# Kernel optimization log

Measured on AMD Instinct MI355X. Metric: run time of the kernel, lower is better.

The kernel has to match this reference:

```python
import jax, jax.numpy as jnp
from jax import lax
import numpy as np

DN = ('NCHW', 'OIHW', 'NCHW')


def conv3x3(x, w, b):
    y = lax.conv_general_dilated(x, w, (1, 1), ((1, 1), (1, 1)), dimension_numbers=DN)
    return y + b[None, :, None, None]


def box_mean(x, k):
    # Uniform k x k box mean with reflect padding; separable (exactly equal to
    # the dense ones/k^2 conv in the original since the kernel is rank-1).
    pad = k // 2
    C = x.shape[1]
    xp = jnp.pad(x, ((0, 0), (0, 0), (pad, pad), (pad, pad)), mode='reflect')
    kh = jnp.ones((C, 1, k, 1), x.dtype) / k
    kw = jnp.ones((C, 1, 1, k), x.dtype) / k
    y = lax.conv_general_dilated(xp, kh, (1, 1), 'VALID', feature_group_count=C, dimension_numbers=DN)
    y = lax.conv_general_dilated(y, kw, (1, 1), 'VALID', feature_group_count=C, dimension_numbers=DN)
    return y


def std_map_for_window(features, k):
    # features: [N, 8, H, W]
    C = features.shape[1]
    m = box_mean(features, k)
    m2 = box_mean(features * features, k)
    var = jnp.maximum(m2 - m * m, 1e-6)
    w = jax.nn.softmax(jnp.ones((C,), features.dtype))  # uniform (C==8 branch)
    sm = jnp.einsum('nchw,c->nhw', jnp.sqrt(var), w)[:, None]  # [N,1,H,W]
    return jnp.power(sm, 0.8)


def setup_inputs() -> dict:
    key = jax.random.key(0)
    ks = jax.random.split(key, 8)
    B, H, W = 8, 512, 512
    x = jax.random.normal(ks[0], (B, 4, H, W), dtype=jnp.float32)
    s = 0.05
    conv1_w = jax.random.normal(ks[1], (32, 4, 3, 3), jnp.float32) * s
    conv1_b = jnp.zeros((32,), jnp.float32)
    conv2_w = jax.random.normal(ks[2], (16, 32, 3, 3), jnp.float32) * s
    conv2_b = jnp.zeros((16,), jnp.float32)
    conv3_w = jax.random.normal(ks[3], (8, 16, 3, 3), jnp.float32) * s
    conv3_b = jnp.zeros((8,), jnp.float32)
    fusion_w = jnp.full((1, 3, 1, 1), 1.0 / 3.0, jnp.float32)  # init per module
    fusion_b = jnp.zeros((1,), jnp.float32)
    channel_weights = jnp.ones((4,), jnp.float32) / 4.0
    return dict(x=x, conv1_w=conv1_w, conv1_b=conv1_b, conv2_w=conv2_w,
                conv2_b=conv2_b, conv3_w=conv3_w, conv3_b=conv3_b,
                fusion_w=fusion_w, fusion_b=fusion_b,
                channel_weights=channel_weights)


def reference(x, conv1_w, conv1_b, conv2_w, conv2_b, conv3_w, conv3_b,
              fusion_w, fusion_b, channel_weights):
    window_sizes = (11, 25, 49)
    # feature extractor
    f = jax.nn.leaky_relu(conv3x3(x, conv1_w, conv1_b), 0.2)
    f = jax.nn.leaky_relu(conv3x3(f, conv2_w, conv2_b), 0.2)
    f = conv3x3(f, conv3_w, conv3_b)  # [B,8,H,W]
    # multi-scale std maps
    maps = [std_map_for_window(f, k) for k in window_sizes]
    multi = jnp.concatenate(maps, axis=1)  # [B,3,H,W]
    fused = jax.nn.relu(
        lax.conv_general_dilated(multi, fusion_w, (1, 1), 'VALID', dimension_numbers=DN)
        + fusion_b[None, :, None, None])  # [B,1,H,W]
    # adaptive thresholds
    std_flat = fused.ravel()
    q = jnp.quantile(std_flat, jnp.array([0.25, 0.75], fused.dtype))
    q25, q75 = q[0], q[1]
    iqr = q75 - q25
    iqr = jnp.where(iqr < 1e-5, jnp.asarray(0.05, fused.dtype), iqr)
    global_std = jnp.std(x, axis=(2, 3), keepdims=True, ddof=1)  # [B,4,1,1]
    lower = jnp.broadcast_to((q25 - 0.5 * iqr), global_std.shape)
    upper = jnp.broadcast_to((q75 + 0.5 * iqr), global_std.shape)
    gf = jnp.clip(global_std * 5.0, 0.5, 2.0)
    lower = lower * gf
    upper = upper * gf
    cw = jax.nn.softmax(channel_weights).reshape(1, 4, 1, 1)
    channel_std = jnp.std(x * cw, axis=(2, 3), keepdims=True, ddof=1)
    cf = jnp.clip(channel_std * 2.0, 0.8, 1.2)
    lower = lower * cf
    upper = upper * cf
    degenerate = jnp.min(jnp.abs(upper - lower)) < 1e-5
    mean_t = (upper + lower) / 2
    lower = jnp.where(degenerate, mean_t - 0.05, lower)
    upper = jnp.where(degenerate, mean_t + 0.05, upper)
    # texture mask
    diff = jnp.maximum(upper - lower, 1e-5)
    norm = jnp.clip((fused - lower) / diff, 0.0, 1.0)  # [B,4,H,W] via broadcast
    mask = jax.nn.sigmoid(6.0 * norm - 3.0)
    return jnp.mean(mask, axis=1, keepdims=True)  # [B,1,H,W]
```

## Files before the change

### kernel.cpp

```cpp
#include <hip/hip_runtime.h>
#include <hip/hip_bf16.h>
#include <math.h>


__global__ __launch_bounds__(256, 2) void conv12_k(
    const float* __restrict__ x,
    const float* __restrict__ w1,
    const float* __restrict__ b1,
    const float* __restrict__ w2,
    const float* __restrict__ b2,
    float* __restrict__ f2)
{
    __shared__ float xs[4 * 36 * 68];
    __shared__ float f1s[4 * 34 * 68];

    const int t  = threadIdx.x;
    const int tx = t & 7;
    const int ty = t >> 3;
    const int x0 = blockIdx.x * 64;
    const int y0 = blockIdx.y * 32;
    const int bb = blockIdx.z;
    const float* xb = x + (size_t)bb * 4 * 262144;

    for (int i = t; i < 9792; i += 256) {
        int ci  = i / 2448;
        int rem = i - ci * 2448;
        int r   = rem / 68;
        int c   = rem - r * 68;
        int Y = y0 - 2 + r, X = x0 - 2 + c;
        float v = 0.f;
        if ((unsigned)Y < 512u && (unsigned)X < 512u)
            v = xb[ci * 262144 + Y * 512 + X];
        xs[i] = v;
    }

    float acc[16][8];
#pragma unroll
    for (int j = 0; j < 16; ++j)
#pragma unroll
        for (int p = 0; p < 8; ++p) acc[j][p] = 0.f;

    for (int g = 0; g < 8; ++g) {
        __syncthreads();

        {
            const int g4 = g * 4;
            for (int it = t; it < 578; it += 256) {
                int r  = it / 17;
                int q  = it - r * 17;
                int c0 = q * 4;
                int Y1 = y0 - 1 + r;
                float v[4][4];
#pragma unroll
                for (int fc = 0; fc < 4; ++fc) {
                    float b = b1[g4 + fc];
                    v[fc][0] = b; v[fc][1] = b; v[fc][2] = b; v[fc][3] = b;
                }
#pragma unroll
                for (int ci = 0; ci < 4; ++ci) {
#pragma unroll
                    for (int ky = 0; ky < 3; ++ky) {
                        const float* xr = &xs[ci * 2448 + (r + ky) * 68 + c0];
                        float4 a  = *(const float4*)xr;
                        float2 bl = *(const float2*)(xr + 4);
                        float rr[6] = {a.x, a.y, a.z, a.w, bl.x, bl.y};
#pragma unroll
                        for (int fc = 0; fc < 4; ++fc) {
#pragma unroll
                            for (int kx = 0; kx < 3; ++kx) {
                                float w = w1[(g4 + fc) * 36 + ci * 9 + ky * 3 + kx];
#pragma unroll
                                for (int p = 0; p < 4; ++p)
                                    v[fc][p] = fmaf(rr[p + kx], w, v[fc][p]);
                            }
                        }
                    }
                }
                bool rowok = ((unsigned)Y1 < 512u);
#pragma unroll
                for (int fc = 0; fc < 4; ++fc) {
                    float st[4];
#pragma unroll
                    for (int p = 0; p < 4; ++p) {
                        int X1 = x0 - 1 + c0 + p;
                        bool ok = rowok && ((unsigned)X1 < 512u) && (c0 + p <= 65);
                        float tv = v[fc][p];
                        tv = tv > 0.f ? tv : 0.2f * tv;
                        st[p] = ok ? tv : 0.f;
                    }
                    *(float4*)&f1s[fc * 2312 + r * 68 + c0] =
                        make_float4(st[0], st[1], st[2], st[3]);
                }
            }
        }
        __syncthreads();

#pragma unroll
        for (int fc = 0; fc < 4; ++fc) {
            const int ci = g * 4 + fc;
#pragma unroll
            for (int dy = 0; dy < 3; ++dy) {
                const float* rowp = &f1s[fc * 2312 + (ty + dy) * 68 + tx * 8];
                float4 a0 = *(const float4*)(rowp);
                float4 a1 = *(const float4*)(rowp + 4);
                float2 a2 = *(const float2*)(rowp + 8);
                float rr[10] = {a0.x, a0.y, a0.z, a0.w,
                                a1.x, a1.y, a1.z, a1.w, a2.x, a2.y};
#pragma unroll
                for (int j = 0; j < 16; ++j) {
#pragma unroll
                    for (int dx = 0; dx < 3; ++dx) {
                        float w = w2[(j * 32 + ci) * 9 + dy * 3 + dx];
#pragma unroll
                        for (int p = 0; p < 8; ++p)
                            acc[j][p] = fmaf(rr[p + dx], w, acc[j][p]);
                    }
                }
            }
        }
    }

    const int y = y0 + ty;
#pragma unroll
    for (int j = 0; j < 16; ++j) {
        float b = b2[j];
        float* op = f2 + (((size_t)bb * 16 + j) * 512 + y) * 512 + x0 + tx * 8;
        float v[8];
#pragma unroll
        for (int p = 0; p < 8; ++p) {
            float tv = acc[j][p] + b;
            v[p] = tv > 0.f ? tv : 0.2f * tv;
        }
        ((float4*)op)[0] = make_float4(v[0], v[1], v[2], v[3]);
        ((float4*)op)[1] = make_float4(v[4], v[5], v[6], v[7]);
    }
}

__global__ __launch_bounds__(256) void conv3_k(
    const float* __restrict__ in,
    const float* __restrict__ wgt,
    const float* __restrict__ bias,
    float* __restrict__ out)
{
    constexpr int TW = 64, TH = 32, SW = TW + 4;
    __shared__ float sl[(TH + 2) * SW];

    const int tx = threadIdx.x & 7;
    const int ty = threadIdx.x >> 3;
    const int x0 = blockIdx.x * TW;
    const int y0 = blockIdx.y * TH;
    const int bb = blockIdx.z;

    const float* inb = in + (size_t)bb * 16 * 262144;

    float acc[8][8];
#pragma unroll
    for (int j = 0; j < 8; ++j)
#pragma unroll
        for (int p = 0; p < 8; ++p) acc[j][p] = 0.f;

    for (int ci = 0; ci < 16; ++ci) {
        __syncthreads();
        const float* ip = inb + (size_t)ci * 262144;
        for (int idx = threadIdx.x; idx < (TH + 2) * (TW + 2); idx += 256) {
            int r  = idx / (TW + 2);
            int cc = idx - r * (TW + 2);
            int yy = y0 - 1 + r, xx = x0 - 1 + cc;
            float v = 0.f;
            if ((unsigned)yy < 512u && (unsigned)xx < 512u) v = ip[yy * 512 + xx];
            sl[r * SW + cc] = v;
        }
        __syncthreads();
        const float* wci = wgt + (size_t)ci * 9;
#pragma unroll
        for (int dy = 0; dy < 3; ++dy) {
            const float* rowp = &sl[(ty + dy) * SW + tx * 8];
            float4 a0 = *(const float4*)(rowp);
            float4 a1 = *(const float4*)(rowp + 4);
            float2 a2 = *(const float2*)(rowp + 8);
            float rr[10] = {a0.x, a0.y, a0.z, a0.w,
                            a1.x, a1.y, a1.z, a1.w, a2.x, a2.y};
#pragma unroll
            for (int j = 0; j < 8; ++j) {
#pragma unroll
                for (int dx = 0; dx < 3; ++dx) {
                    float w = wci[(size_t)j * 16 * 9 + dy * 3 + dx];
#pragma unroll
                    for (int p = 0; p < 8; ++p)
                        acc[j][p] = fmaf(rr[p + dx], w, acc[j][p]);
                }
            }
        }
    }

    const int y = y0 + ty;
#pragma unroll
    for (int j = 0; j < 8; ++j) {
        float b = bias[j];
        float* op = out + (((size_t)bb * 8 + j) * 512 + y) * 512 + x0 + tx * 8;
        float v[8];
#pragma unroll
        for (int p = 0; p < 8; ++p) v[p] = acc[j][p] + b;
        ((float4*)op)[0] = make_float4(v[0], v[1], v[2], v[3]);
        ((float4*)op)[1] = make_float4(v[4], v[5], v[6], v[7]);
    }
}

__device__ __forceinline__ float2 f2add(float2 a, float2 b) {
    return make_float2(a.x + b.x, a.y + b.y);
}
__device__ __forceinline__ int mir(int v) {
    return v < 0 ? -v : (v > 511 ? 1022 - v : v);
}

#define YB 4

__global__ __launch_bounds__(256) void stdmap_k(
    const float* __restrict__ f,
    const float* __restrict__ fw,
    const float* __restrict__ fbp,
    float* __restrict__ fused,
    int b0)
{
    const int total = gridDim.x * gridDim.y;
    const int lin   = blockIdx.y * gridDim.x + blockIdx.x;
    const int task  = (lin & 7) * (total >> 3) + (lin >> 3);
    const int bb    = task >> 7;
    const int y0    = (task & 127) * YB;
    const int t    = threadIdx.x;
    const int lane = t & 63, wid = t >> 6;

    __shared__ float S[3][2][513];
    __shared__ float wtt[4][6];

    const int   RAD[3] = {5, 12, 24};
    const float INV[3] = {1.f/121.f, 1.f/625.f, 1.f/2401.f};

    float smacc[3][YB][2];
#pragma unroll
    for (int sc = 0; sc < 3; ++sc)
#pragma unroll
        for (int yy = 0; yy < YB; ++yy)
            { smacc[sc][yy][0] = 0.f; smacc[sc][yy][1] = 0.f; }

    for (int c = 0; c < 8; ++c) {
        const float* base = f + ((size_t)bb * 8 + c) * 512 * 512;

        float2 wf[3], wq[3];
        {
            float2 sf[3] = {{0.f,0.f},{0.f,0.f},{0.f,0.f}};
            float2 sq[3] = {{0.f,0.f},{0.f,0.f},{0.f,0.f}};
#pragma unroll
            for (int dy = -24; dy <= 24; ++dy) {
                int row = mir(y0 + dy);
                float2 v  = ((const float2*)(base + (size_t)row * 512))[t];
                float2 vq = make_float2(v.x * v.x, v.y * v.y);
                int ad = dy < 0 ? -dy : dy;
                int ring = ad <= 5 ? 0 : (ad <= 12 ? 1 : 2);
                sf[ring] = f2add(sf[ring], v);
                sq[ring] = f2add(sq[ring], vq);
            }
            wf[0] = sf[0];               wq[0] = sq[0];
            wf[1] = f2add(sf[1], wf[0]); wq[1] = f2add(sq[1], wq[0]);
            wf[2] = f2add(sf[2], wf[1]); wq[2] = f2add(sq[2], wq[1]);
        }

        for (int yy = 0; yy < YB; ++yy) {
            const int y = y0 + yy;
            if (yy > 0) {
#pragma unroll
                for (int sc = 0; sc < 3; ++sc) {
                    int ra = mir(y + RAD[sc]);
                    int rs = mir(y - 1 - RAD[sc]);
                    float2 va = ((const float2*)(base + (size_t)ra * 512))[t];
                    float2 vs = ((const float2*)(base + (size_t)rs * 512))[t];
                    wf[sc].x += va.x - vs.x;       wf[sc].y += va.y - vs.y;
                    wq[sc].x += va.x*va.x - vs.x*vs.x;
                    wq[sc].y += va.y*va.y - vs.y*vs.y;
                }
            }

            float pf[3], pq[3], incf[3], incq[3];
#pragma unroll
            for (int sc = 0; sc < 3; ++sc) {
                pf[sc] = wf[sc].x + wf[sc].y;
                pq[sc] = wq[sc].x + wq[sc].y;
                incf[sc] = pf[sc]; incq[sc] = pq[sc];
            }
#pragma unroll
            for (int off = 1; off < 64; off <<= 1) {
#pragma unroll
                for (int sc = 0; sc < 3; ++sc) {
                    float uf = __shfl_up(incf[sc], (unsigned)off, 64);
                    float uq = __shfl_up(incq[sc], (unsigned)off, 64);
                    if (lane >= off) { incf[sc] += uf; incq[sc] += uq; }
                }
            }
            if (lane == 63) {
#pragma unroll
                for (int sc = 0; sc < 3; ++sc) {
                    wtt[wid][sc]     = incf[sc];
                    wtt[wid][3 + sc] = incq[sc];
                }
            }
            __syncthreads();
            float wpf[3] = {0.f,0.f,0.f}, wpq[3] = {0.f,0.f,0.f};
#pragma unroll
            for (int w = 0; w < 4; ++w)
                if (w < wid)
#pragma unroll
                    for (int sc = 0; sc < 3; ++sc) {
                        wpf[sc] += wtt[w][sc];
                        wpq[sc] += wtt[w][3 + sc];
                    }
#pragma unroll
            for (int sc = 0; sc < 3; ++sc) {
                float exf = wpf[sc] + incf[sc] - pf[sc];
                float exq = wpq[sc] + incq[sc] - pq[sc];
                S[sc][0][2*t+1] = exf + wf[sc].x;
                S[sc][0][2*t+2] = exf + pf[sc];
                S[sc][1][2*t+1] = exq + wq[sc].x;
                S[sc][1][2*t+2] = exq + pq[sc];
            }
            if (t == 0)
#pragma unroll
                for (int sc = 0; sc < 3; ++sc)
                    { S[sc][0][0] = 0.f; S[sc][1][0] = 0.f; }
            __syncthreads();

#pragma unroll
            for (int sc = 0; sc < 3; ++sc) {
                const int r = RAD[sc];
                const float* Sf = S[sc][0];
                const float* Sq = S[sc][1];
#pragma unroll
                for (int slot = 0; slot < 2; ++slot) {
                    int xx = 2*t + slot;
                    int lo = xx - r, hi = xx + r;
                    int loc = lo < 0 ? 0 : lo;
                    int hic = hi > 511 ? 511 : hi;
                    float wfv = Sf[hic + 1] - Sf[loc];
                    float wqv = Sq[hic + 1] - Sq[loc];
                    if (lo < 0)   { wfv += Sf[r - xx + 1] - Sf[1];
                                    wqv += Sq[r - xx + 1] - Sq[1]; }
                    if (hi > 511) { wfv += Sf[511] - Sf[1022 - xx - r];
                                    wqv += Sq[511] - Sq[1022 - xx - r]; }
                    float m   = wfv * INV[sc];
                    float m2  = wqv * INV[sc];
                    float var = m2 - m * m;
                    var = var > 1e-6f ? var : 1e-6f;
                    smacc[sc][yy][slot] += sqrtf(var);
                }
            }
            __syncthreads();
        }
    }

    const float w0 = fw[0], w1 = fw[1], w2 = fw[2], b = fbp[0];
#pragma unroll
    for (int yy = 0; yy < YB; ++yy) {
        float o[2];
#pragma unroll
        for (int slot = 0; slot < 2; ++slot) {
            float m0 = powf(smacc[0][yy][slot] * 0.125f, 0.8f);
            float m1 = powf(smacc[1][yy][slot] * 0.125f, 0.8f);
            float m2 = powf(smacc[2][yy][slot] * 0.125f, 0.8f);
            float fv = w0 * m0 + w1 * m1 + w2 * m2 + b;
            o[slot] = fv > 0.f ? fv : 0.f;
        }
        ((float2*)(fused + ((size_t)(b0 + bb) * 512 + y0 + yy) * 512))[t] =
            make_float2(o[0], o[1]);
    }
}

__global__ __launch_bounds__(256) void plane_std_part_k(
    const float* __restrict__ x, double* __restrict__ part)
{
    const int plane = blockIdx.x >> 5;
    const int blk   = blockIdx.x & 31;
    const float* p = x + (size_t)plane * 262144 + (size_t)blk * 8192;
    double s = 0.0, s2 = 0.0;
    for (int i = threadIdx.x; i < 2048; i += 256) {
        float4 v = ((const float4*)p)[i];
        s  += (double)v.x + (double)v.y + (double)v.z + (double)v.w;
        s2 += (double)v.x * v.x + (double)v.y * v.y
            + (double)v.z * v.z + (double)v.w * v.w;
    }
    __shared__ double ls[256], ls2[256];
    ls[threadIdx.x] = s; ls2[threadIdx.x] = s2;
    __syncthreads();
    for (int off = 128; off > 0; off >>= 1) {
        if (threadIdx.x < off) {
            ls[threadIdx.x]  += ls[threadIdx.x + off];
            ls2[threadIdx.x] += ls2[threadIdx.x + off];
        }
        __syncthreads();
    }
    if (threadIdx.x == 0) {
        part[2 * blockIdx.x]     = ls[0];
        part[2 * blockIdx.x + 1] = ls2[0];
    }
}

__global__ void plane_std_fin_k(const double* __restrict__ part,
                                float* __restrict__ stds)
{
    const int plane = threadIdx.x;
    if (plane >= 32) return;
    double s = 0.0, s2 = 0.0;
    for (int b = 0; b < 32; ++b) {
        s  += part[2 * (plane * 32 + b)];
        s2 += part[2 * (plane * 32 + b) + 1];
    }
    const double N = 262144.0;
    double var = (s2 - s * s / N) / (N - 1.0);
    stds[plane] = (float)sqrt(var > 0.0 ? var : 0.0);
}

__global__ __launch_bounds__(256) void hist1_k(
    const float* __restrict__ fused, unsigned* __restrict__ h)
{
    __shared__ unsigned lh[4096];
    for (int i = threadIdx.x; i < 4096; i += 256) lh[i] = 0u;
    __syncthreads();
    const int base = blockIdx.x * 2048;
    for (int i = threadIdx.x; i < 2048; i += 256) {
        unsigned bits = __float_as_uint(fused[base + i]);
        atomicAdd(&lh[bits >> 20], 1u);
    }
    __syncthreads();
    for (int i = threadIdx.x; i < 4096; i += 256) {
        unsigned c = lh[i];
        if (c) atomicAdd(&h[i], c);
    }
}

__global__ __launch_bounds__(256) void select_par_k(
    const unsigned* __restrict__ h, unsigned* __restrict__ pfx,
    unsigned* __restrict__ rem, int level)
{
    const int tt = blockIdx.x;
    const int t = threadIdx.x, lane = t & 63, wid = t >> 6;
    const unsigned targets[4] = {524287u, 524288u, 1572863u, 1572864u};
    const unsigned R = (level == 1) ? targets[tt] : rem[tt];
    const unsigned* hb = (level == 1) ? h : h + tt * 4096;

    unsigned loc[16], lsum = 0;
    const uint4* hv = (const uint4*)(hb + t * 16);
#pragma unroll
    for (int i = 0; i < 4; ++i) {
        uint4 v = hv[i];
        loc[4*i]=v.x; loc[4*i+1]=v.y; loc[4*i+2]=v.z; loc[4*i+3]=v.w;
        lsum += v.x + v.y + v.z + v.w;
    }
    __shared__ unsigned warr[4];
    __shared__ unsigned rbin, rrem;
    unsigned inc = lsum;
#pragma unroll
    for (int off = 1; off < 64; off <<= 1) {
        unsigned up = __shfl_up(inc, (unsigned)off, 64);
        if (lane >= off) inc += up;
    }
    if (lane == 63) warr[wid] = inc;
    __syncthreads();
    unsigned wpre = 0;
#pragma unroll
    for (int w = 0; w < 4; ++w) if (w < wid) wpre += warr[w];
    unsigned ex = wpre + inc - lsum;
    if (R >= ex && R < ex + lsum) {
        unsigned cum = ex;
#pragma unroll
        for (int i = 0; i < 16; ++i) {
            if (cum + loc[i] > R) { rbin = (unsigned)(t * 16 + i); rrem = R - cum; break; }
            cum += loc[i];
        }
    }
    __syncthreads();
    if (t == 0) {
        if (level == 1) { pfx[tt] = rbin << 20; rem[tt] = rrem; }
        else            { pfx[tt] |= rbin << 8; rem[tt] = rrem; }
    }
}

__global__ __launch_bounds__(256) void hist2_k(
    const float* __restrict__ fused, const unsigned* __restrict__ pfx,
    unsigned* __restrict__ h2)
{
    __shared__ unsigned lh[4 * 4096];
    for (int i = threadIdx.x; i < 4 * 4096; i += 256) lh[i] = 0u;
    unsigned p0 = pfx[0] >> 20, p1 = pfx[1] >> 20,
             p2 = pfx[2] >> 20, p3 = pfx[3] >> 20;
    __syncthreads();
    const int base = blockIdx.x * 2048;
    for (int i = threadIdx.x; i < 2048; i += 256) {
        unsigned bits = __float_as_uint(fused[base + i]);
        unsigned top = bits >> 20;
        unsigned mid = (bits >> 8) & 0xFFFu;
        if (top == p0) atomicAdd(&lh[0 * 4096 + mid], 1u);
        if (top == p1) atomicAdd(&lh[1 * 4096 + mid], 1u);
        if (top == p2) atomicAdd(&lh[2 * 4096 + mid], 1u);
        if (top == p3) atomicAdd(&lh[3 * 4096 + mid], 1u);
    }
    __syncthreads();
    for (int i = threadIdx.x; i < 4 * 4096; i += 256) {
        unsigned c = lh[i];
        if (c) atomicAdd(&h2[i], c);
    }
}

__global__ __launch_bounds__(256) void hist3_k(
    const float* __restrict__ fused, const unsigned* __restrict__ pfx,
    unsigned* __restrict__ h3)
{
    __shared__ unsigned lh[4 * 256];
    for (int i = threadIdx.x; i < 4 * 256; i += 256) lh[i] = 0u;
    unsigned p0 = pfx[0] >> 8, p1 = pfx[1] >> 8,
             p2 = pfx[2] >> 8, p3 = pfx[3] >> 8;
    __syncthreads();
    const int base = blockIdx.x * 2048;
    for (int i = threadIdx.x; i < 2048; i += 256) {
        unsigned bits = __float_as_uint(fused[base + i]);
        unsigned top = bits >> 8;
        unsigned low = bits & 0xFFu;
        if (top == p0) atomicAdd(&lh[0 * 256 + low], 1u);
        if (top == p1) atomicAdd(&lh[1 * 256 + low], 1u);
        if (top == p2) atomicAdd(&lh[2 * 256 + low], 1u);
        if (top == p3) atomicAdd(&lh[3 * 256 + low], 1u);
    }
    __syncthreads();
    for (int i = threadIdx.x; i < 4 * 256; i += 256) {
        unsigned c = lh[i];
        if (c) atomicAdd(&h3[i], c);
    }
}

__device__ __forceinline__ float clampf(float v, float lo, float hi) {
    return v < lo ? lo : (v > hi ? hi : v);
}

__global__ __launch_bounds__(256) void finalize_k(
    const unsigned* __restrict__ h3,
    const unsigned* __restrict__ pfx,
    const unsigned* __restrict__ rem,
    const float* __restrict__ stds,
    const float* __restrict__ cw,
    float* __restrict__ lu)
{
    const int tt = threadIdx.x >> 6, lane = threadIdx.x & 63;
    __shared__ float vals[4];

    {
        const unsigned R = rem[tt];
        const unsigned* h = h3 + tt * 256;
        uint4 v = ((const uint4*)h)[lane];
        unsigned loc[4] = {v.x, v.y, v.z, v.w};
        unsigned lsum = v.x + v.y + v.z + v.w;
        unsigned inc = lsum;
#pragma unroll
        for (int off = 1; off < 64; off <<= 1) {
            unsigned up = __shfl_up(inc, (unsigned)off, 64);
            if (lane >= off) inc += up;
        }
        unsigned ex = inc - lsum;
        if (R >= ex && R < ex + lsum) {
            unsigned cum = ex;
#pragma unroll
            for (int i = 0; i < 4; ++i) {
                if (cum + loc[i] > R) {
                    vals[tt] = __uint_as_float(pfx[tt] | (unsigned)(lane * 4 + i));
                    break;
                }
                cum += loc[i];
            }
        }
    }
    __syncthreads();
    if (threadIdx.x != 0) return;

    float q25 = vals[0] + 0.75f * (vals[1] - vals[0]);
    float q75 = vals[2] + 0.25f * (vals[3] - vals[2]);
    float iqr = q75 - q25;
    if (iqr < 1e-5f) iqr = 0.05f;
    float lo0 = q25 - 0.5f * iqr, up0 = q75 + 0.5f * iqr;

    float mx = cw[0];
    for (int c = 1; c < 4; ++c) mx = cw[c] > mx ? cw[c] : mx;
    float e[4], se = 0.f;
    for (int c = 0; c < 4; ++c) { e[c] = expf(cw[c] - mx); se += e[c]; }

    float l[32], u[32], mind = 1e30f;
    for (int p = 0; p < 32; ++p) {
        float sd = stds[p];
        int c = p & 3;
        float gf = clampf(sd * 5.f, 0.5f, 2.f);
        float cf = clampf(sd * (e[c] / se) * 2.f, 0.8f, 1.2f);
        l[p] = lo0 * gf * cf;
        u[p] = up0 * gf * cf;
        float d = fabsf(u[p] - l[p]);
        if (d < mind) mind = d;
    }
    bool deg = mind < 1e-5f;
    for (int p = 0; p < 32; ++p) {
        float L = l[p], U = u[p];
        if (deg) { float m = 0.5f * (L + U); L = m - 0.05f; U = m + 0.05f; }
        lu[p] = L; lu[32 + p] = U;
    }
}

__global__ __launch_bounds__(256) void mask_k(
    const float* __restrict__ fused, const float* __restrict__ lu,
    float* __restrict__ out)
{
    const int b = blockIdx.y;
    const int i = blockIdx.x * 256 + threadIdx.x;
    float fv = fused[(size_t)b * 262144 + i];
    float s = 0.f;
#pragma unroll
    for (int c = 0; c < 4; ++c) {
        float L = lu[b * 4 + c], U = lu[32 + b * 4 + c];
        float d = U - L; d = d > 1e-5f ? d : 1e-5f;
        float n = (fv - L) / d;
        n = n < 0.f ? 0.f : (n > 1.f ? 1.f : n);
        s += 1.f / (1.f + expf(3.f - 6.f * n));
    }
    out[(size_t)b * 262144 + i] = 0.25f * s;
}

extern "C" void kernel_launch(void* const* d_in, const int* in_sizes, int n_in,
                              void* d_out, int out_size, void* d_ws, size_t ws_size,
                              hipStream_t stream)
{
    const float* x   = (const float*)d_in[0];
    const float* c1w = (const float*)d_in[1];
    const float* c1b = (const float*)d_in[2];
    const float* c2w = (const float*)d_in[3];
    const float* c2b = (const float*)d_in[4];
    const float* c3w = (const float*)d_in[5];
    const float* c3b = (const float*)d_in[6];
    const float* fw  = (const float*)d_in[7];
    const float* fb  = (const float*)d_in[8];
    const float* cwt = (const float*)d_in[9];
    float* out = (float*)d_out;
    char* ws = (char*)d_ws;

    const size_t PLANE = 512 * 512;

    float* fused = (float*)ws;
    size_t off = 8 * PLANE * sizeof(float);
    float* stds = (float*)(ws + off); off += 32 * 4;
    float* lu   = (float*)(ws + off); off += 64 * 4;
    off = (off + 255) & ~(size_t)255;
    unsigned* pfx = (unsigned*)(ws + off); off += 16;
    unsigned* rem = (unsigned*)(ws + off); off += 16;
    off = (off + 255) & ~(size_t)255;
    unsigned* h1 = (unsigned*)(ws + off); off += 4096 * 4;
    unsigned* h2 = (unsigned*)(ws + off); off += 4 * 4096 * 4;
    unsigned* h3 = (unsigned*)(ws + off); off += 4 * 256 * 4;
    off = (off + 255) & ~(size_t)255;
    double* part = (double*)(ws + off); off += 1024 * 2 * sizeof(double);
    off = (off + 1023) & ~(size_t)1023;

    const size_t perb = 24 * PLANE * sizeof(float);
    int nb = 8;
    while (nb > 1 && off + (size_t)nb * perb > ws_size) nb >>= 1;
    float* f2  = (float*)(ws + off);
    float* fch = f2 + (size_t)nb * 16 * PLANE;

    hipLaunchKernelGGL(plane_std_part_k, dim3(1024), dim3(256), 0, stream, x, part);
    hipLaunchKernelGGL(plane_std_fin_k,  dim3(1),    dim3(64),  0, stream, part, stds);

    for (int b0 = 0; b0 < 8; b0 += nb) {
        const float* xc = x + (size_t)b0 * 4 * PLANE;
        hipLaunchKernelGGL(conv12_k, dim3(8, 16, nb), dim3(256), 0, stream,
                           xc, c1w, c1b, c2w, c2b, f2);
        hipLaunchKernelGGL(conv3_k,  dim3(8, 16, nb), dim3(256), 0, stream,
                           f2, c3w, c3b, fch);
        hipLaunchKernelGGL(stdmap_k, dim3(512 / YB, nb), dim3(256), 0, stream,
                           fch, fw, fb, fused, b0);
    }

    hipMemsetAsync(h1, 0, (4096 + 4 * 4096 + 4 * 256) * 4, stream);
    hipLaunchKernelGGL(hist1_k,     dim3(1024), dim3(256), 0, stream, fused, h1);
    hipLaunchKernelGGL(select_par_k, dim3(4),   dim3(256), 0, stream, h1, pfx, rem, 1);
    hipLaunchKernelGGL(hist2_k,     dim3(1024), dim3(256), 0, stream, fused, pfx, h2);
    hipLaunchKernelGGL(select_par_k, dim3(4),   dim3(256), 0, stream, h2, pfx, rem, 2);
    hipLaunchKernelGGL(hist3_k,     dim3(1024), dim3(256), 0, stream, fused, pfx, h3);
    hipLaunchKernelGGL(finalize_k,  dim3(1),    dim3(256), 0, stream,
                       h3, pfx, rem, stds, cwt, lu);
    hipLaunchKernelGGL(mask_k, dim3(1024, 8), dim3(256), 0, stream, fused, lu, out);
}
```

Before: 1.095 ms.

## Use zero-padded global buffers for conv inputs and batch conv3 channel staging

Adds a kernel that copies x into zero-padded planes and another that zeroes the halo of a padded f2 buffer. conv12 then reads x straight from global memory instead of staging it in shared memory, and writes f2 into the padded layout. conv3 stages four input channels per sync with vectorized, branch-free loads instead of one channel at a time. The aim is to remove bounds checks, cut shared-memory use and reduce barriers, at the cost of two extra kernels, extra workspace, and uncached-style global reads inside conv12's inner loop.

Result: slower. 1.186 ms (+8.3%).

```diff
diff --git a/kernel.cpp b/kernel.cpp
--- a/kernel.cpp
+++ b/kernel.cpp
@@ -3,15 +3,56 @@
 #include <math.h>
 
 
+#define XP_H 516
+#define XP_W 528
+#define F2P_H 514
+#define F2P_W 528
+
+__global__ __launch_bounds__(256) void pad_x_k(
+    const float* __restrict__ x, float* __restrict__ xp, int nplanes)
+{
+    const int i = blockIdx.x * 256 + threadIdx.x;
+    const int PER = XP_H * (XP_W / 4);
+    if (i >= nplanes * PER) return;
+    const int pl  = i / PER;
+    const int rem = i - pl * PER;
+    const int r   = rem / (XP_W / 4);
+    const int q   = rem - r * (XP_W / 4);
+    float4 v = make_float4(0.f, 0.f, 0.f, 0.f);
+    if (r >= 2 && r < 514 && q >= 2 && q < 130)
+        v = ((const float4*)(x + (size_t)pl * 262144 + (size_t)(r - 2) * 512))[q - 2];
+    ((float4*)(xp + (size_t)pl * XP_H * XP_W + (size_t)r * XP_W))[q] = v;
+}
+
+__global__ __launch_bounds__(256) void zero_f2p_k(
+    float* __restrict__ f2p, int nplanes)
+{
+    const int PER = 132 + 132 + 512 * 4;
+    const int i = blockIdx.x * 256 + threadIdx.x;
+    if (i >= nplanes * PER) return;
+    const int pl = i / PER;
+    int e = i - pl * PER;
+    int r, q;
+    if (e < 132)       { r = 0;   q = e; }
+    else if (e < 264)  { r = 513; q = e - 132; }
+    else {
+        e -= 264;
+        r = 1 + (e >> 2);
+        int idx = e & 3;
+        q = idx < 2 ? idx : 128 + idx;
+    }
+    ((float4*)(f2p + (size_t)pl * F2P_H * F2P_W + (size_t)r * F2P_W))[q] =
+        make_float4(0.f, 0.f, 0.f, 0.f);
+}
+
 __global__ __launch_bounds__(256, 2) void conv12_k(
-    const float* __restrict__ x,
+    const float* __restrict__ xp,
     const float* __restrict__ w1,
     const float* __restrict__ b1,
     const float* __restrict__ w2,
     const float* __restrict__ b2,
-    float* __restrict__ f2)
-{
-    __shared__ float xs[4 * 36 * 68];
+    float* __restrict__ f2p)
+{
     __shared__ float f1s[4 * 34 * 68];
 
     const int t  = threadIdx.x;
@@ -20,19 +61,7 @@
     const int x0 = blockIdx.x * 64;
     const int y0 = blockIdx.y * 32;
     const int bb = blockIdx.z;
-    const float* xb = x + (size_t)bb * 4 * 262144;
-
-    for (int i = t; i < 9792; i += 256) {
-        int ci  = i / 2448;
-        int rem = i - ci * 2448;
-        int r   = rem / 68;
-        int c   = rem - r * 68;
-        int Y = y0 - 2 + r, X = x0 - 2 + c;
-        float v = 0.f;
-        if ((unsigned)Y < 512u && (unsigned)X < 512u)
-            v = xb[ci * 262144 + Y * 512 + X];
-        xs[i] = v;
-    }
+    const float* xpb = xp + (size_t)(bb * 4) * XP_H * XP_W;
 
     float acc[16][8];
 #pragma unroll
@@ -60,10 +89,13 @@
                 for (int ci = 0; ci < 4; ++ci) {
 #pragma unroll
                     for (int ky = 0; ky < 3; ++ky) {
-                        const float* xr = &xs[ci * 2448 + (r + ky) * 68 + c0];
-                        float4 a  = *(const float4*)xr;
-                        float2 bl = *(const float2*)(xr + 4);
-                        float rr[6] = {a.x, a.y, a.z, a.w, bl.x, bl.y};
+                        const float* xr = xpb + (size_t)ci * XP_H * XP_W
+                                        + (size_t)(y0 + r + ky) * XP_W
+                                        + x0 + 6 + c0;
+                        float2 A = *(const float2*)xr;
+                        float2 B = *(const float2*)(xr + 2);
+                        float2 C = *(const float2*)(xr + 4);
+                        float rr[6] = {A.x, A.y, B.x, B.y, C.x, C.y};
 #pragma unroll
                         for (int fc = 0; fc < 4; ++fc) {
 #pragma unroll
@@ -124,7 +156,8 @@
 #pragma unroll
     for (int j = 0; j < 16; ++j) {
         float b = b2[j];
-        float* op = f2 + (((size_t)bb * 16 + j) * 512 + y) * 512 + x0 + tx * 8;
+        float* op = f2p + ((size_t)(bb * 16 + j) * F2P_H + (y + 1)) * F2P_W
+                  + x0 + 8 + tx * 8;
         float v[8];
 #pragma unroll
         for (int p = 0; p < 8; ++p) {
@@ -137,57 +170,66 @@
 }
 
 __global__ __launch_bounds__(256) void conv3_k(
-    const float* __restrict__ in,
+    const float* __restrict__ f2p,
     const float* __restrict__ wgt,
     const float* __restrict__ bias,
     float* __restrict__ out)
 {
-    constexpr int TW = 64, TH = 32, SW = TW + 4;
-    __shared__ float sl[(TH + 2) * SW];
-
-    const int tx = threadIdx.x & 7;
-    const int ty = threadIdx.x >> 3;
-    const int x0 = blockIdx.x * TW;
-    const int y0 = blockIdx.y * TH;
+    __shared__ float sl[4 * 34 * 72];
+
+    const int t  = threadIdx.x;
+    const int tx = t & 7;
+    const int ty = t >> 3;
+    const int x0 = blockIdx.x * 64;
+    const int y0 = blockIdx.y * 32;
     const int bb = blockIdx.z;
 
-    const float* inb = in + (size_t)bb * 16 * 262144;
-
     float acc[8][8];
 #pragma unroll
     for (int j = 0; j < 8; ++j)
 #pragma unroll
         for (int p = 0; p < 8; ++p) acc[j][p] = 0.f;
 
-    for (int ci = 0; ci < 16; ++ci) {
+    for (int cg = 0; cg < 4; ++cg) {
         __syncthreads();
-        const float* ip = inb + (size_t)ci * 262144;
-        for (int idx = threadIdx.x; idx < (TH + 2) * (TW + 2); idx += 256) {
-            int r  = idx / (TW + 2);
-            int cc = idx - r * (TW + 2);
-            int yy = y0 - 1 + r, xx = x0 - 1 + cc;
-            float v = 0.f;
-            if ((unsigned)yy < 512u && (unsigned)xx < 512u) v = ip[yy * 512 + xx];
-            sl[r * SW + cc] = v;
+        for (int i = t; i < 2448; i += 256) {
+            int ch  = i / 612;
+            int rem = i - ch * 612;
+            int rr  = rem / 18;
+            int s   = rem - rr * 18;
+            const float* src = f2p
+                + ((size_t)(bb * 16 + cg * 4 + ch) * F2P_H + (y0 + rr)) * F2P_W
+                + x0;
+            float* dst = &sl[ch * 2448 + rr * 72];
+            if (s == 16)      dst[0]  = src[7];
+            else if (s == 17) dst[65] = src[72];
+            else {
+                float4 v = *(const float4*)(src + 8 + s * 4);
+                dst[4*s+1] = v.x; dst[4*s+2] = v.y;
+                dst[4*s+3] = v.z; dst[4*s+4] = v.w;
+            }
         }
         __syncthreads();
-        const float* wci = wgt + (size_t)ci * 9;
-#pragma unroll
-        for (int dy = 0; dy < 3; ++dy) {
-            const float* rowp = &sl[(ty + dy) * SW + tx * 8];
-            float4 a0 = *(const float4*)(rowp);
-            float4 a1 = *(const float4*)(rowp + 4);
-            float2 a2 = *(const float2*)(rowp + 8);
-            float rr[10] = {a0.x, a0.y, a0.z, a0.w,
-                            a1.x, a1.y, a1.z, a1.w, a2.x, a2.y};
-#pragma unroll
-            for (int j = 0; j < 8; ++j) {
-#pragma unroll
-                for (int dx = 0; dx < 3; ++dx) {
-                    float w = wci[(size_t)j * 16 * 9 + dy * 3 + dx];
-#pragma unroll
-                    for (int p = 0; p < 8; ++p)
-                        acc[j][p] = fmaf(rr[p + dx], w, acc[j][p]);
+#pragma unroll
+        for (int ci = 0; ci < 4; ++ci) {
+            const int cig = cg * 4 + ci;
+#pragma unroll
+            for (int dy = 0; dy < 3; ++dy) {
+                const float* rowp = &sl[ci * 2448 + (ty + dy) * 72 + tx * 8];
+                float4 a0 = *(const float4*)(rowp);
+                float4 a1 = *(const float4*)(rowp + 4);
+                float2 a2 = *(const float2*)(rowp + 8);
+                float rr[10] = {a0.x, a0.y, a0.z, a0.w,
+                                a1.x, a1.y, a1.z, a1.w, a2.x, a2.y};
+#pragma unroll
+                for (int j = 0; j < 8; ++j) {
+#pragma unroll
+                    for (int dx = 0; dx < 3; ++dx) {
+                        float w = wgt[((size_t)j * 16 + cig) * 9 + dy * 3 + dx];
+#pragma unroll
+                        for (int p = 0; p < 8; ++p)
+                            acc[j][p] = fmaf(rr[p + dx], w, acc[j][p]);
+                    }
                 }
             }
         }
@@ -660,21 +702,32 @@
     double* part = (double*)(ws + off); off += 1024 * 2 * sizeof(double);
     off = (off + 1023) & ~(size_t)1023;
 
-    const size_t perb = 24 * PLANE * sizeof(float);
+    const size_t xp_pb  = (size_t)4 * XP_H * XP_W;
+    const size_t f2p_pb = (size_t)16 * F2P_H * F2P_W;
+    const size_t perb = (xp_pb + f2p_pb + 8 * PLANE) * sizeof(float);
     int nb = 8;
     while (nb > 1 && off + (size_t)nb * perb > ws_size) nb >>= 1;
-    float* f2  = (float*)(ws + off);
-    float* fch = f2 + (size_t)nb * 16 * PLANE;
+    float* xp  = (float*)(ws + off);
+    float* f2p = xp + (size_t)nb * xp_pb;
+    float* fch = f2p + (size_t)nb * f2p_pb;
 
     hipLaunchKernelGGL(plane_std_part_k, dim3(1024), dim3(256), 0, stream, x, part);
     hipLaunchKernelGGL(plane_std_fin_k,  dim3(1),    dim3(64),  0, stream, part, stds);
 
     for (int b0 = 0; b0 < 8; b0 += nb) {
         const float* xc = x + (size_t)b0 * 4 * PLANE;
+        const int xplanes  = nb * 4;
+        const int f2planes = nb * 16;
+        const int padx_items = xplanes * XP_H * (XP_W / 4);
+        const int zf2_items  = f2planes * 2312;
+        hipLaunchKernelGGL(pad_x_k, dim3((padx_items + 255) / 256), dim3(256),
+                           0, stream, xc, xp, xplanes);
+        hipLaunchKernelGGL(zero_f2p_k, dim3((zf2_items + 255) / 256), dim3(256),
+                           0, stream, f2p, f2planes);
         hipLaunchKernelGGL(conv12_k, dim3(8, 16, nb), dim3(256), 0, stream,
-                           xc, c1w, c1b, c2w, c2b, f2);
+                           xp, c1w, c1b, c2w, c2b, f2p);
         hipLaunchKernelGGL(conv3_k,  dim3(8, 16, nb), dim3(256), 0, stream,
-                           f2, c3w, c3b, fch);
+                           f2p, c3w, c3b, fch);
         hipLaunchKernelGGL(stdmap_k, dim3(512 / YB, nb), dim3(256), 0, stream,
                            fch, fw, fb, fused, b0);
     }
```

## Fuse conv1, conv2 and conv3 into one tiled kernel with halo recompute

Applied to the files above, without the earlier changes.

Merges the conv1+conv2 kernel and the separate conv3 kernel into a single kernel. conv2 outputs for the tile plus a one-pixel halo stay in registers and are staged through shared memory, so the 16-channel intermediate no longer goes through global memory. The cost is recomputing the halo for conv1 and conv2 (38x72 input and 36x72 conv1 tiles), 192 accumulator registers per thread (acc[3][16][4]) and extra synchronisation, which may lower occupancy or cause spills.

New measurement: 1.591 ms. 45.3% more time.

```diff
diff --git a/kernel.cpp b/kernel.cpp
--- a/kernel.cpp
+++ b/kernel.cpp
@@ -3,72 +3,76 @@
 #include <math.h>
 
 
-__global__ __launch_bounds__(256, 2) void conv12_k(
+__global__ __launch_bounds__(256, 2) void conv123_k(
     const float* __restrict__ x,
     const float* __restrict__ w1,
     const float* __restrict__ b1,
     const float* __restrict__ w2,
     const float* __restrict__ b2,
-    float* __restrict__ f2)
-{
-    __shared__ float xs[4 * 36 * 68];
-    __shared__ float f1s[4 * 34 * 68];
+    const float* __restrict__ w3,
+    const float* __restrict__ b3,
+    float* __restrict__ fout)
+{
+    __shared__ float xs[4 * 38 * 72 + 8];
+    __shared__ float f1s[2 * 36 * 72];
 
     const int t  = threadIdx.x;
-    const int tx = t & 7;
-    const int ty = t >> 3;
-    const int x0 = blockIdx.x * 64;
-    const int y0 = blockIdx.y * 32;
+    const int tx = t & 7, ty = t >> 3;
+    const int x0 = blockIdx.x * 64, y0 = blockIdx.y * 32;
     const int bb = blockIdx.z;
     const float* xb = x + (size_t)bb * 4 * 262144;
 
-    for (int i = t; i < 9792; i += 256) {
-        int ci  = i / 2448;
-        int rem = i - ci * 2448;
-        int r   = rem / 68;
-        int c   = rem - r * 68;
-        int Y = y0 - 2 + r, X = x0 - 2 + c;
+    for (int i = t; i < 4 * 38 * 72; i += 256) {
+        int ci  = i / (38 * 72);
+        int rem = i - ci * (38 * 72);
+        int r   = rem / 72, c = rem - r * 72;
+        int Y = y0 - 3 + r, X = x0 - 4 + c;
         float v = 0.f;
         if ((unsigned)Y < 512u && (unsigned)X < 512u)
             v = xb[ci * 262144 + Y * 512 + X];
         xs[i] = v;
     }
-
-    float acc[16][8];
-#pragma unroll
-    for (int j = 0; j < 16; ++j)
-#pragma unroll
-        for (int p = 0; p < 8; ++p) acc[j][p] = 0.f;
-
-    for (int g = 0; g < 8; ++g) {
+    if (t < 8) xs[4 * 38 * 72 + t] = 0.f;
+
+    float acc[3][16][4];
+#pragma unroll
+    for (int s = 0; s < 3; ++s)
+#pragma unroll
+        for (int j = 0; j < 16; ++j)
+#pragma unroll
+            for (int p = 0; p < 4; ++p) acc[s][j][p] = 0.f;
+
+    for (int g = 0; g < 16; ++g) {
         __syncthreads();
-
-        {
-            const int g4 = g * 4;
-            for (int it = t; it < 578; it += 256) {
-                int r  = it / 17;
-                int q  = it - r * 17;
+        const int g2 = g * 2;
+
+#pragma unroll
+        for (int s = 0; s < 3; ++s) {
+            int it = t + s * 256;
+            if (it < 648) {
+                int r  = it / 18, q = it - r * 18;
                 int c0 = q * 4;
-                int Y1 = y0 - 1 + r;
-                float v[4][4];
-#pragma unroll
-                for (int fc = 0; fc < 4; ++fc) {
-                    float b = b1[g4 + fc];
+                int Y1 = y0 - 2 + r;
+                float v[2][4];
+#pragma unroll
+                for (int fc = 0; fc < 2; ++fc) {
+                    float b = b1[g2 + fc];
                     v[fc][0] = b; v[fc][1] = b; v[fc][2] = b; v[fc][3] = b;
                 }
 #pragma unroll
                 for (int ci = 0; ci < 4; ++ci) {
 #pragma unroll
                     for (int ky = 0; ky < 3; ++ky) {
-                        const float* xr = &xs[ci * 2448 + (r + ky) * 68 + c0];
-                        float4 a  = *(const float4*)xr;
-                        float2 bl = *(const float2*)(xr + 4);
-                        float rr[6] = {a.x, a.y, a.z, a.w, bl.x, bl.y};
-#pragma unroll
-                        for (int fc = 0; fc < 4; ++fc) {
+                        const float* xr = &xs[ci * 2736 + (r + ky) * 72 + c0];
+                        float2 A = *(const float2*)xr;
+                        float2 B = *(const float2*)(xr + 2);
+                        float2 C = *(const float2*)(xr + 4);
+                        float rr[6] = {A.x, A.y, B.x, B.y, C.x, C.y};
+#pragma unroll
+                        for (int fc = 0; fc < 2; ++fc) {
 #pragma unroll
                             for (int kx = 0; kx < 3; ++kx) {
-                                float w = w1[(g4 + fc) * 36 + ci * 9 + ky * 3 + kx];
+                                float w = w1[(g2 + fc) * 36 + ci * 9 + ky * 3 + kx];
 #pragma unroll
                                 for (int p = 0; p < 4; ++p)
                                     v[fc][p] = fmaf(rr[p + kx], w, v[fc][p]);
@@ -78,17 +82,16 @@
                 }
                 bool rowok = ((unsigned)Y1 < 512u);
 #pragma unroll
-                for (int fc = 0; fc < 4; ++fc) {
+                for (int fc = 0; fc < 2; ++fc) {
                     float st[4];
 #pragma unroll
                     for (int p = 0; p < 4; ++p) {
-                        int X1 = x0 - 1 + c0 + p;
-                        bool ok = rowok && ((unsigned)X1 < 512u) && (c0 + p <= 65);
+                        int X1 = x0 - 3 + c0 + p;
                         float tv = v[fc][p];
                         tv = tv > 0.f ? tv : 0.2f * tv;
-                        st[p] = ok ? tv : 0.f;
+                        st[p] = (rowok && (unsigned)X1 < 512u) ? tv : 0.f;
                     }
-                    *(float4*)&f1s[fc * 2312 + r * 68 + c0] =
+                    *(float4*)&f1s[fc * 2592 + r * 72 + c0] =
                         make_float4(st[0], st[1], st[2], st[3]);
                 }
             }
@@ -96,111 +99,104 @@
         __syncthreads();
 
 #pragma unroll
-        for (int fc = 0; fc < 4; ++fc) {
-            const int ci = g * 4 + fc;
+        for (int s = 0; s < 3; ++s) {
+            int it = t + s * 256;
+            if (it < 578) {
+                int r  = it / 17, q = it - r * 17;
+                int c0 = q * 4;
+#pragma unroll
+                for (int fc = 0; fc < 2; ++fc) {
+                    const int ciw = g2 + fc;
+#pragma unroll
+                    for (int dy = 0; dy < 3; ++dy) {
+                        const float* fp = &f1s[fc * 2592 + (r + dy) * 72 + c0];
+                        float4 A = *(const float4*)fp;
+                        float2 B = *(const float2*)(fp + 4);
+                        float rr[6] = {A.x, A.y, A.z, A.w, B.x, B.y};
+#pragma unroll
+                        for (int j = 0; j < 16; ++j) {
+#pragma unroll
+                            for (int dx = 0; dx < 3; ++dx) {
+                                float w = w2[(j * 32 + ciw) * 9 + dy * 3 + dx];
+#pragma unroll
+                                for (int p = 0; p < 4; ++p)
+                                    acc[s][j][p] = fmaf(rr[p + dx], w, acc[s][j][p]);
+                            }
+                        }
+                    }
+                }
+            }
+        }
+    }
+
+    float acc3[8][8];
+#pragma unroll
+    for (int j = 0; j < 8; ++j)
+#pragma unroll
+        for (int p = 0; p < 8; ++p) acc3[j][p] = 0.f;
+
+    float* f2s = xs;
+    for (int cg = 0; cg < 4; ++cg) {
+#pragma unroll
+        for (int s = 0; s < 3; ++s) {
+            int it = t + s * 256;
+            if (it < 578) {
+                int r  = it / 17, q = it - r * 17;
+                int c0 = q * 4;
+                int Y2 = y0 - 1 + r;
+                bool rok = ((unsigned)Y2 < 512u);
+#pragma unroll
+                for (int c2 = 0; c2 < 4; ++c2) {
+                    int jj = cg * 4 + c2;
+                    float b = b2[jj];
+                    float st[4];
+#pragma unroll
+                    for (int p = 0; p < 4; ++p) {
+                        int X2 = x0 - 2 + c0 + p;
+                        float tv = acc[s][jj][p] + b;
+                        tv = tv > 0.f ? tv : 0.2f * tv;
+                        st[p] = (rok && (unsigned)X2 < 512u) ? tv : 0.f;
+                    }
+                    *(float4*)&f2s[c2 * 2448 + r * 72 + c0] =
+                        make_float4(st[0], st[1], st[2], st[3]);
+                }
+            }
+        }
+        __syncthreads();
+#pragma unroll
+        for (int c2 = 0; c2 < 4; ++c2) {
+            const int ci = cg * 4 + c2;
 #pragma unroll
             for (int dy = 0; dy < 3; ++dy) {
-                const float* rowp = &f1s[fc * 2312 + (ty + dy) * 68 + tx * 8];
-                float4 a0 = *(const float4*)(rowp);
-                float4 a1 = *(const float4*)(rowp + 4);
-                float2 a2 = *(const float2*)(rowp + 8);
-                float rr[10] = {a0.x, a0.y, a0.z, a0.w,
-                                a1.x, a1.y, a1.z, a1.w, a2.x, a2.y};
-#pragma unroll
-                for (int j = 0; j < 16; ++j) {
+                const float* fp = &f2s[c2 * 2448 + (ty + dy) * 72 + tx * 8];
+                float4 A = ((const float4*)fp)[0];
+                float4 B = ((const float4*)fp)[1];
+                float4 C = ((const float4*)fp)[2];
+                float rr[12] = {A.x, A.y, A.z, A.w, B.x, B.y, B.z, B.w,
+                                C.x, C.y, C.z, C.w};
+#pragma unroll
+                for (int j = 0; j < 8; ++j) {
 #pragma unroll
                     for (int dx = 0; dx < 3; ++dx) {
-                        float w = w2[(j * 32 + ci) * 9 + dy * 3 + dx];
+                        float w = w3[(j * 16 + ci) * 9 + dy * 3 + dx];
 #pragma unroll
                         for (int p = 0; p < 8; ++p)
-                            acc[j][p] = fmaf(rr[p + dx], w, acc[j][p]);
+                            acc3[j][p] = fmaf(rr[p + dx + 1], w, acc3[j][p]);
                     }
                 }
             }
         }
+        __syncthreads();
     }
 
     const int y = y0 + ty;
 #pragma unroll
-    for (int j = 0; j < 16; ++j) {
-        float b = b2[j];
-        float* op = f2 + (((size_t)bb * 16 + j) * 512 + y) * 512 + x0 + tx * 8;
+    for (int j = 0; j < 8; ++j) {
+        float b = b3[j];
+        float* op = fout + (((size_t)bb * 8 + j) * 512 + y) * 512 + x0 + tx * 8;
         float v[8];
 #pragma unroll
-        for (int p = 0; p < 8; ++p) {
-            float tv = acc[j][p] + b;
-            v[p] = tv > 0.f ? tv : 0.2f * tv;
-        }
-        ((float4*)op)[0] = make_float4(v[0], v[1], v[2], v[3]);
-        ((float4*)op)[1] = make_float4(v[4], v[5], v[6], v[7]);
-    }
-}
-
-__global__ __launch_bounds__(256) void conv3_k(
-    const float* __restrict__ in,
-    const float* __restrict__ wgt,
-    const float* __restrict__ bias,
-    float* __restrict__ out)
-{
-    constexpr int TW = 64, TH = 32, SW = TW + 4;
-    __shared__ float sl[(TH + 2) * SW];
-
-    const int tx = threadIdx.x & 7;
-    const int ty = threadIdx.x >> 3;
-    const int x0 = blockIdx.x * TW;
-    const int y0 = blockIdx.y * TH;
-    const int bb = blockIdx.z;
-
-    const float* inb = in + (size_t)bb * 16 * 262144;
-
-    float acc[8][8];
-#pragma unroll
-    for (int j = 0; j < 8; ++j)
-#pragma unroll
-        for (int p = 0; p < 8; ++p) acc[j][p] = 0.f;
-
-    for (int ci = 0; ci < 16; ++ci) {
-        __syncthreads();
-        const float* ip = inb + (size_t)ci * 262144;
-        for (int idx = threadIdx.x; idx < (TH + 2) * (TW + 2); idx += 256) {
-            int r  = idx / (TW + 2);
-            int cc = idx - r * (TW + 2);
-            int yy = y0 - 1 + r, xx = x0 - 1 + cc;
-            float v = 0.f;
-            if ((unsigned)yy < 512u && (unsigned)xx < 512u) v = ip[yy * 512 + xx];
-            sl[r * SW + cc] = v;
-        }
-        __syncthreads();
-        const float* wci = wgt + (size_t)ci * 9;
-#pragma unroll
-        for (int dy = 0; dy < 3; ++dy) {
-            const float* rowp = &sl[(ty + dy) * SW + tx * 8];
-            float4 a0 = *(const float4*)(rowp);
-            float4 a1 = *(const float4*)(rowp + 4);
-            float2 a2 = *(const float2*)(rowp + 8);
-            float rr[10] = {a0.x, a0.y, a0.z, a0.w,
-                            a1.x, a1.y, a1.z, a1.w, a2.x, a2.y};
-#pragma unroll
-            for (int j = 0; j < 8; ++j) {
-#pragma unroll
-                for (int dx = 0; dx < 3; ++dx) {
-                    float w = wci[(size_t)j * 16 * 9 + dy * 3 + dx];
-#pragma unroll
-                    for (int p = 0; p < 8; ++p)
-                        acc[j][p] = fmaf(rr[p + dx], w, acc[j][p]);
-                }
-            }
-        }
-    }
-
-    const int y = y0 + ty;
-#pragma unroll
-    for (int j = 0; j < 8; ++j) {
-        float b = bias[j];
-        float* op = out + (((size_t)bb * 8 + j) * 512 + y) * 512 + x0 + tx * 8;
-        float v[8];
-#pragma unroll
-        for (int p = 0; p < 8; ++p) v[p] = acc[j][p] + b;
+        for (int p = 0; p < 8; ++p) v[p] = acc3[j][p] + b;
         ((float4*)op)[0] = make_float4(v[0], v[1], v[2], v[3]);
         ((float4*)op)[1] = make_float4(v[4], v[5], v[6], v[7]);
     }
@@ -660,21 +656,18 @@
     double* part = (double*)(ws + off); off += 1024 * 2 * sizeof(double);
     off = (off + 1023) & ~(size_t)1023;
 
-    const size_t perb = 24 * PLANE * sizeof(float);
+    const size_t perb = 8 * PLANE * sizeof(float);
     int nb = 8;
     while (nb > 1 && off + (size_t)nb * perb > ws_size) nb >>= 1;
-    float* f2  = (float*)(ws + off);
-    float* fch = f2 + (size_t)nb * 16 * PLANE;
+    float* fch = (float*)(ws + off);
 
     hipLaunchKernelGGL(plane_std_part_k, dim3(1024), dim3(256), 0, stream, x, part);
     hipLaunchKernelGGL(plane_std_fin_k,  dim3(1),    dim3(64),  0, stream, part, stds);
 
     for (int b0 = 0; b0 < 8; b0 += nb) {
         const float* xc = x + (size_t)b0 * 4 * PLANE;
-        hipLaunchKernelGGL(conv12_k, dim3(8, 16, nb), dim3(256), 0, stream,
-                           xc, c1w, c1b, c2w, c2b, f2);
-        hipLaunchKernelGGL(conv3_k,  dim3(8, 16, nb), dim3(256), 0, stream,
-                           f2, c3w, c3b, fch);
+        hipLaunchKernelGGL(conv123_k, dim3(8, 16, nb), dim3(256), 0, stream,
+                           xc, c1w, c1b, c2w, c2b, c3w, c3b, fch);
         hipLaunchKernelGGL(stdmap_k, dim3(512 / YB, nb), dim3(256), 0, stream,
                            fch, fw, fb, fused, b0);
     }
```
